# Performance work log

Measured on AMD Instinct MI355X. Metric: run time of the kernel, lower is better.

## Reference

```python
import jax, jax.numpy as jnp
import numpy as np

B, NS, NT = 4, 512, 512
D_IN, C1, R, C2 = 128, 64, 32, 32
E = 32768
STEPS = 10


def setup_inputs() -> dict:
    key = jax.random.key(0)
    ks = jax.random.split(key, 12)
    inp = {}
    inp['x_s'] = jax.random.normal(ks[0], (B * NS, D_IN), jnp.float32)
    inp['edge_index_s'] = jax.random.randint(ks[1], (2, E), 0, B * NS, jnp.int32)
    inp['edge_attr_s'] = jax.random.uniform(ks[2], (E,), jnp.float32)
    inp['batch_s'] = (jnp.arange(B * NS, dtype=jnp.int32) // NS)
    inp['x_t'] = jax.random.normal(ks[3], (B * NT, D_IN), jnp.float32)
    inp['edge_index_t'] = jax.random.randint(ks[4], (2, E), 0, B * NT, jnp.int32)
    inp['edge_attr_t'] = jax.random.uniform(ks[5], (E,), jnp.float32)
    inp['batch_t'] = (jnp.arange(B * NT, dtype=jnp.int32) // NT)
    inp['W1'] = jax.random.normal(ks[6], (D_IN, C1), jnp.float32) / np.float32(np.sqrt(D_IN))
    inp['W2'] = jax.random.normal(ks[7], (R, C2), jnp.float32) / np.float32(np.sqrt(R))
    inp['mw1'] = jax.random.normal(ks[8], (C2, C2), jnp.float32) / np.float32(np.sqrt(C2))
    inp['mb1'] = jnp.zeros((C2,), jnp.float32)
    inp['mw2'] = jax.random.normal(ks[9], (C2, 1), jnp.float32) / np.float32(np.sqrt(C2))
    inp['mb2'] = jnp.zeros((1,), jnp.float32)
    inp['r'] = jax.random.normal(ks[10], (STEPS, B, NS, R), jnp.float32)
    return inp


def psi(x, src, dst, ea, W, n):
    # simple message-passing GNN: edge-weighted neighbor aggregation + linear + ReLU
    m = jax.ops.segment_sum(x[src] * ea[:, None], dst, num_segments=n)
    return jax.nn.relu((x + m) @ W)


def reference(x_s, edge_index_s, edge_attr_s, batch_s, x_t, edge_index_t, edge_attr_t,
              batch_t, W1, W2, mw1, mb1, mw2, mb2, r):
    # Uniform graph sizes -> to_dense_batch is a reshape and all masks are True,
    # so masked_softmax reduces to plain softmax; batch_s/batch_t kept for interface fidelity.
    ss, ds = edge_index_s[0], edge_index_s[1]
    st, dt = edge_index_t[0], edge_index_t[1]
    h_s = psi(x_s, ss, ds, edge_attr_s, W1, B * NS).reshape(B, NS, C1)
    h_t = psi(x_t, st, dt, edge_attr_t, W1, B * NT).reshape(B, NT, C1)
    S_hat0 = jnp.einsum('bsc,btc->bst', h_s, h_t)  # [B, NS, NT]
    S_0 = jax.nn.softmax(S_hat0, axis=-1)

    def step(S_hat, r_i):
        S = jax.nn.softmax(S_hat, axis=-1)
        r_t = jnp.einsum('bst,bsr->btr', S, r_i)  # S^T @ r_s
        o_s = psi(r_i.reshape(B * NS, R), ss, ds, edge_attr_s, W2, B * NS).reshape(B, NS, C2)
        o_t = psi(r_t.reshape(B * NT, R), st, dt, edge_attr_t, W2, B * NT).reshape(B, NT, C2)
        Dm = o_s[:, :, None, :] - o_t[:, None, :, :]  # [B, NS, NT, C2] outer difference
        upd = (jax.nn.relu(Dm @ mw1 + mb1) @ mw2 + mb2)[..., 0]
        return S_hat + upd, None

    S_hat, _ = jax.lax.scan(step, S_hat0, r)
    S_L = jax.nn.softmax(S_hat, axis=-1)
    return (S_0, S_L)
```

## Files before the change

kernel.cpp:

```cpp
#include <hip/hip_runtime.h>


constexpr int kB = 4;
constexpr int kNS = 512;
constexpr int kNT = 512;
constexpr int kDin = 128;
constexpr int kC1 = 64;
constexpr int kR = 32;
constexpr int kC2 = 32;
constexpr int kE = 32768;
constexpr int kSteps = 10;
constexpr int kN = kB * kNS;
constexpr int kEP = kE + 16 * kN;
constexpr int kChunkStride = kR * kN;

__global__ void k_hist(const int* __restrict__ ei_s, const int* __restrict__ ei_t,
                       int* __restrict__ deg) {
  int g = blockIdx.y;
  const int* dst = (g ? ei_t : ei_s) + kE;
  int e = blockIdx.x * 256 + threadIdx.x;
  atomicAdd(&deg[g * kN + dst[e]], 1);
}

__global__ void k_scan(const int* __restrict__ deg, int* __restrict__ off,
                       int* __restrict__ cur) {
  int g = blockIdx.x;
  const int* d = deg + g * kN;
  int* o = off + g * (kN + 1);
  int* c = cur + g * kN;
  __shared__ int sums[256];
  int tid = threadIdx.x;
  int loc[8];
  int s = 0;
#pragma unroll
  for (int i = 0; i < 8; ++i) {
    loc[i] = (d[tid * 8 + i] + 15) & ~15;
    s += loc[i];
  }
  sums[tid] = s;
  __syncthreads();
  for (int st = 1; st < 256; st <<= 1) {
    int v = (tid >= st) ? sums[tid - st] : 0;
    __syncthreads();
    sums[tid] += v;
    __syncthreads();
  }
  int base = (tid > 0) ? sums[tid - 1] : 0;
#pragma unroll
  for (int i = 0; i < 8; ++i) {
    int idx = tid * 8 + i;
    o[idx] = base;
    c[idx] = base;
    base += loc[i];
  }
  if (tid == 255) o[kN] = base;
}

__global__ void k_scatter(const int* __restrict__ ei_s, const int* __restrict__ ei_t,
                          const float* __restrict__ ea_s, const float* __restrict__ ea_t,
                          int* __restrict__ cur, int* __restrict__ srcs,
                          float* __restrict__ eaw) {
  int g = blockIdx.y;
  const int* ei = g ? ei_t : ei_s;
  const float* ea = g ? ea_t : ea_s;
  int e = blockIdx.x * 256 + threadIdx.x;
  int d = ei[kE + e];
  int srcv = ei[e];
  int pos = atomicAdd(&cur[g * kN + d], 1);
  srcs[g * kEP + pos] = srcv;
  eaw[g * kEP + pos] = ea[e];
}

__device__ __forceinline__ void psi2_node(
    int n, const float* __restrict__ vin, const int* __restrict__ sr,
    const float* __restrict__ ew, const int* __restrict__ o,
    const float* __restrict__ W2, const float* __restrict__ mw1,
    const float* __restrict__ mb1, float* __restrict__ Pout) {
  int lane = threadIdx.x & 63;
  int f = lane & 31, hh = lane >> 5;
  int beg = o[n], end = o[n + 1];
  float m = 0.f;
  for (int b0 = beg + hh * 8; b0 < end; b0 += 16) {
#pragma unroll
    for (int q = 0; q < 8; ++q)
      m += vin[(size_t)sr[b0 + q] * kR + f] * ew[b0 + q];
  }
  m += __shfl_down(m, 32, 64);
  float v = vin[(size_t)n * kR + f] + m;
  float acc = 0.f;
#pragma unroll
  for (int k = 0; k < kC2; ++k) acc += __shfl(v, k, 64) * W2[k * kC2 + f];
  float ov = fmaxf(acc, 0.f);
  float p = mb1 ? mb1[f] : 0.f;
#pragma unroll
  for (int k = 0; k < kC2; ++k) p += __shfl(ov, k, 64) * mw1[k * kC2 + f];
  if (lane < 32) Pout[(size_t)n * kC2 + f] = p;
}

__global__ __launch_bounds__(256) void k_pre(
    const float* __restrict__ x_s, const float* __restrict__ x_t,
    const float* __restrict__ r, const int* __restrict__ srcs,
    const float* __restrict__ eaw, const int* __restrict__ off,
    const float* __restrict__ W1, const float* __restrict__ W2,
    const float* __restrict__ mw1, const float* __restrict__ mb1,
    float* __restrict__ h, float* __restrict__ PsAll) {
  int bid = blockIdx.x, tid = threadIdx.x;
  if (bid < 2048) {
    int g = bid >> 10;
    int n = (bid & 1023) * 2 + (tid >> 7);
    int f = tid & 127;
    const float* x = g ? x_t : x_s;
    const int* sr = srcs + g * kEP;
    const float* ew = eaw + g * kEP;
    const int* o = off + g * (kN + 1);
    float* ho = h + (size_t)g * kN * kC1;
    __shared__ float y[2][kDin];
    int beg = o[n], end = o[n + 1];
    float xself = x[(size_t)n * kDin + f];
    float m = 0.f;
    for (int idx = beg; idx < end; idx += 8) {
      float a0 = x[(size_t)sr[idx + 0] * kDin + f] * ew[idx + 0];
      float a1 = x[(size_t)sr[idx + 1] * kDin + f] * ew[idx + 1];
      float a2 = x[(size_t)sr[idx + 2] * kDin + f] * ew[idx + 2];
      float a3 = x[(size_t)sr[idx + 3] * kDin + f] * ew[idx + 3];
      float a4 = x[(size_t)sr[idx + 4] * kDin + f] * ew[idx + 4];
      float a5 = x[(size_t)sr[idx + 5] * kDin + f] * ew[idx + 5];
      float a6 = x[(size_t)sr[idx + 6] * kDin + f] * ew[idx + 6];
      float a7 = x[(size_t)sr[idx + 7] * kDin + f] * ew[idx + 7];
      m += ((a0 + a1) + (a2 + a3)) + ((a4 + a5) + (a6 + a7));
    }
    y[tid >> 7][f] = xself + m;
    __syncthreads();
    if (f < kC1) {
      const float* yy = y[tid >> 7];
      float acc = 0.f;
#pragma unroll 16
      for (int k = 0; k < kDin; ++k) acc += yy[k] * W1[k * kC1 + f];
      ho[(size_t)n * kC1 + f] = fmaxf(acc, 0.f);
    }
  } else {
    int nn = (bid - 2048) * 4 + (tid >> 6);
    int step = nn >> 11, node = nn & (kN - 1);
    psi2_node(node, r + (size_t)step * kN * kR, srcs, eaw, off, W2, mw1, mb1,
              PsAll + (size_t)step * kN * kR);
  }
}

__global__ __launch_bounds__(256) void k_shat0(const float* __restrict__ h,
                                               float* __restrict__ Shat,
                                               float* __restrict__ pstatm,
                                               float* __restrict__ pstatl) {
  int b = blockIdx.z, s0 = blockIdx.y * 64, t0 = blockIdx.x * 64;
  const float* hs = h + (size_t)(b * kNS + s0) * kC1;
  const float* ht = h + (size_t)kN * kC1 + (size_t)(b * kNT + t0) * kC1;
  __shared__ float As[64 * 68];
  __shared__ float Bs[64 * 68];
  int tid = threadIdx.x;
#pragma unroll
  for (int k2 = 0; k2 < 4; ++k2) {
    int idx = tid + k2 * 256;
    int row = idx >> 4, c4 = idx & 15;
    float4 va = *(const float4*)(hs + (size_t)row * kC1 + c4 * 4);
    *(float4*)&As[row * 68 + c4 * 4] = va;
    float4 vb = *(const float4*)(ht + (size_t)row * kC1 + c4 * 4);
    *(float4*)&Bs[row * 68 + c4 * 4] = vb;
  }
  __syncthreads();
  int ts = tid >> 4, tt = tid & 15;
  float acc[4][4] = {};
#pragma unroll
  for (int cc = 0; cc < 16; ++cc) {
    float4 a[4], bt[4];
#pragma unroll
    for (int i = 0; i < 4; ++i) a[i] = *(const float4*)&As[(ts * 4 + i) * 68 + cc * 4];
#pragma unroll
    for (int k = 0; k < 4; ++k) bt[k] = *(const float4*)&Bs[(tt + 16 * k) * 68 + cc * 4];
#pragma unroll
    for (int i = 0; i < 4; ++i)
#pragma unroll
      for (int k = 0; k < 4; ++k)
        acc[i][k] += a[i].x * bt[k].x + a[i].y * bt[k].y + a[i].z * bt[k].z + a[i].w * bt[k].w;
  }
#pragma unroll
  for (int i = 0; i < 4; ++i) {
    int s = s0 + ts * 4 + i;
    float* row = Shat + (size_t)(b * kNS + s) * kNT;
#pragma unroll
    for (int k = 0; k < 4; ++k) row[t0 + tt + 16 * k] = acc[i][k];
  }
#pragma unroll
  for (int i = 0; i < 4; ++i) {
    float mm = fmaxf(fmaxf(acc[i][0], acc[i][1]), fmaxf(acc[i][2], acc[i][3]));
#pragma unroll
    for (int o2 = 8; o2; o2 >>= 1) mm = fmaxf(mm, __shfl_xor(mm, o2, 64));
    float se = 0.f;
#pragma unroll
    for (int k = 0; k < 4; ++k) se += __expf(acc[i][k] - mm);
#pragma unroll
    for (int o2 = 8; o2; o2 >>= 1) se += __shfl_xor(se, o2, 64);
    if (tt == 0) {
      int grow = b * kNS + s0 + ts * 4 + i;
      pstatm[blockIdx.x * kN + grow] = mm;
      pstatl[blockIdx.x * kN + grow] = se;
    }
  }
}

__global__ __launch_bounds__(256) void k_rt(const float* __restrict__ Shat,
                                            const float* __restrict__ pstatm,
                                            const float* __restrict__ pstatl,
                                            const float* __restrict__ ri,
                                            float* __restrict__ part, int nc,
                                            float* __restrict__ Sout) {
  int b = blockIdx.z, cs = blockIdx.y, s0 = cs * 64, t0 = blockIdx.x * 32;
  __shared__ float Wt[64 * 32];
  __shared__ float rch[64 * 32];
  __shared__ float lm[64], ll[64];
  int tid = threadIdx.x;
  if (tid < 64) {
    int row = b * kNS + s0 + tid;
    float m = -3.4e38f;
    for (int c = 0; c < nc; ++c) m = fmaxf(m, pstatm[c * kN + row]);
    float l = 0.f;
    for (int c = 0; c < nc; ++c) l += __expf(pstatm[c * kN + row] - m) * pstatl[c * kN + row];
    lm[tid] = m;
    ll[tid] = 1.f / l;
  }
  __syncthreads();
#pragma unroll
  for (int k2 = 0; k2 < 2; ++k2) {
    int idx = tid + k2 * 256;
    int row = idx >> 3, c4 = idx & 7;
    int grow = b * kNS + s0 + row;
    float4 v = *(const float4*)(Shat + (size_t)grow * kNT + t0 + c4 * 4);
    float m = lm[row], l = ll[row];
    float4 wv;
    wv.x = __expf(v.x - m) * l;
    wv.y = __expf(v.y - m) * l;
    wv.z = __expf(v.z - m) * l;
    wv.w = __expf(v.w - m) * l;
    *(float4*)&Wt[row * 32 + c4 * 4] = wv;
    if (Sout) *(float4*)(Sout + (size_t)grow * kNT + t0 + c4 * 4) = wv;
    float4 rv = *(const float4*)(ri + (size_t)grow * kR + c4 * 4);
    *(float4*)&rch[row * 32 + c4 * 4] = rv;
  }
  __syncthreads();
  int t_l = tid & 31, jg = tid >> 5;
  float4 acc = make_float4(0.f, 0.f, 0.f, 0.f);
  for (int s = 0; s < 64; ++s) {
    float wv = Wt[s * 32 + t_l];
    float4 rv = *(const float4*)&rch[s * 32 + jg * 4];
    acc.x += wv * rv.x; acc.y += wv * rv.y; acc.z += wv * rv.z; acc.w += wv * rv.w;
  }
  int gcol = b * kNT + t0 + t_l;
  float* dst = part + (size_t)cs * kChunkStride + (size_t)jg * 4 * kN + gcol;
  dst[0] = acc.x;
  dst[(size_t)kN] = acc.y;
  dst[(size_t)2 * kN] = acc.z;
  dst[(size_t)3 * kN] = acc.w;
}

__global__ __launch_bounds__(256) void k_red(const float* __restrict__ part,
                                             float* __restrict__ rt) {
  int idx = blockIdx.x * 256 + threadIdx.x;
  int j = idx >> 11, col = idx & (kN - 1);
  float s = 0.f;
#pragma unroll
  for (int cs = 0; cs < 8; ++cs) s += part[(size_t)cs * kChunkStride + idx];
  rt[(size_t)col * kR + j] = s;
}

__global__ __launch_bounds__(256) void k_psi2t(
    const float* __restrict__ rt, const int* __restrict__ srcs,
    const float* __restrict__ eaw, const int* __restrict__ off,
    const float* __restrict__ W2, const float* __restrict__ mw1,
    float* __restrict__ Pt) {
  int n = blockIdx.x * 4 + (threadIdx.x >> 6);
  psi2_node(n, rt, srcs + kEP, eaw + kEP, off + (kN + 1), W2, mw1, nullptr, Pt);
}

__global__ __launch_bounds__(256) void k_upd(
    float* __restrict__ Shat, const float* __restrict__ Ps,
    const float* __restrict__ Pt, const float* __restrict__ mw2,
    const float* __restrict__ mb2, float* __restrict__ pstatm,
    float* __restrict__ pstatl) {
  __shared__ float pts[256 * 33];
  __shared__ float red[8 * 4];
  __shared__ float lmx[8];
  int tid = threadIdx.x;
  int g0 = blockIdx.x * 8;
  int cc = blockIdx.y;
  int bb = g0 >> 9;
  int c0 = cc * 256;
  const float4* PtB = (const float4*)(Pt + ((size_t)bb * kNT + c0) * kC2);
#pragma unroll
  for (int k = 0; k < 8; ++k) {
    int idx = tid + k * 256;
    int col = idx >> 3, q = idx & 7;
    float4 v = PtB[idx];
    float* d = &pts[col * 33 + q * 4];
    d[0] = v.x; d[1] = v.y; d[2] = v.z; d[3] = v.w;
  }
  float old[8];
#pragma unroll
  for (int s = 0; s < 8; ++s) old[s] = Shat[(size_t)(g0 + s) * kNT + c0 + tid];
  __syncthreads();
  float pt[32];
#pragma unroll
  for (int j = 0; j < 32; ++j) pt[j] = pts[tid * 33 + j];
  float bias = mb2[0];
  float nv[8];
#pragma unroll
  for (int s = 0; s < 8; ++s) {
    const float* psr = Ps + (size_t)(g0 + s) * kC2;
    float u = 0.f;
#pragma unroll
    for (int j = 0; j < 32; ++j) u += fmaxf(psr[j] - pt[j], 0.f) * mw2[j];
    float v = old[s] + u + bias;
    Shat[(size_t)(g0 + s) * kNT + c0 + tid] = v;
    nv[s] = v;
  }
  int wv = tid >> 6, ln = tid & 63;
#pragma unroll
  for (int s = 0; s < 8; ++s) {
    float m = nv[s];
#pragma unroll
    for (int o2 = 32; o2; o2 >>= 1) m = fmaxf(m, __shfl_down(m, o2, 64));
    if (ln == 0) red[s * 4 + wv] = m;
  }
  __syncthreads();
  if (tid < 8) {
    lmx[tid] = fmaxf(fmaxf(red[tid * 4], red[tid * 4 + 1]),
                     fmaxf(red[tid * 4 + 2], red[tid * 4 + 3]));
  }
  __syncthreads();
#pragma unroll
  for (int s = 0; s < 8; ++s) {
    float e = __expf(nv[s] - lmx[s]);
#pragma unroll
    for (int o2 = 32; o2; o2 >>= 1) e += __shfl_down(e, o2, 64);
    if (ln == 0) red[s * 4 + wv] = e;
  }
  __syncthreads();
  if (tid < 8) {
    float l = red[tid * 4] + red[tid * 4 + 1] + red[tid * 4 + 2] + red[tid * 4 + 3];
    pstatm[cc * kN + g0 + tid] = lmx[tid];
    pstatl[cc * kN + g0 + tid] = l;
  }
}

__global__ __launch_bounds__(256) void k_out(const float* __restrict__ Shat,
                                             const float* __restrict__ pstatm,
                                             const float* __restrict__ pstatl,
                                             float* __restrict__ out) {
  int row = blockIdx.x, tid = threadIdx.x;
  float m0 = pstatm[row], m1 = pstatm[kN + row];
  float l0 = pstatl[row], l1 = pstatl[kN + row];
  float m = fmaxf(m0, m1);
  float linv = 1.f / (__expf(m0 - m) * l0 + __expf(m1 - m) * l1);
  const float* p = Shat + (size_t)row * kNT;
  float* d = out + (size_t)row * kNT;
  d[tid] = __expf(p[tid] - m) * linv;
  d[tid + 256] = __expf(p[tid + 256] - m) * linv;
}

extern "C" void kernel_launch(void* const* d_in, const int* in_sizes, int n_in,
                              void* d_out, int out_size, void* d_ws, size_t ws_size,
                              hipStream_t stream) {
  (void)in_sizes; (void)n_in; (void)out_size; (void)ws_size;
  const float* x_s = (const float*)d_in[0];
  const int* ei_s = (const int*)d_in[1];
  const float* ea_s = (const float*)d_in[2];
  const float* x_t = (const float*)d_in[4];
  const int* ei_t = (const int*)d_in[5];
  const float* ea_t = (const float*)d_in[6];
  const float* W1 = (const float*)d_in[8];
  const float* W2 = (const float*)d_in[9];
  const float* mw1 = (const float*)d_in[10];
  const float* mb1 = (const float*)d_in[11];
  const float* mw2 = (const float*)d_in[12];
  const float* mb2 = (const float*)d_in[13];
  const float* r = (const float*)d_in[14];
  float* out = (float*)d_out;

  char* w = (char*)d_ws;
  auto alloc = [&](size_t bytes) -> void* {
    void* p = (void*)w;
    w += (bytes + 255) & ~(size_t)255;
    return p;
  };
  int* deg = (int*)alloc((size_t)2 * kN * 4);
  int* cur = (int*)alloc((size_t)2 * kN * 4);
  int* srcs = (int*)alloc((size_t)2 * kEP * 4);
  float* eaw = (float*)alloc((size_t)2 * kEP * 4);
  size_t zbytes = (size_t)((char*)(eaw + 2 * kEP) - (char*)deg);
  int* off = (int*)alloc((size_t)2 * (kN + 1) * 4);
  float* h = (float*)alloc((size_t)2 * kN * kC1 * 4);
  float* Shat = (float*)alloc((size_t)kB * kNS * kNT * 4);
  float* pstatm = (float*)alloc((size_t)8 * kN * 4);
  float* pstatl = (float*)alloc((size_t)8 * kN * 4);
  float* rt = (float*)alloc((size_t)kN * kR * 4);
  float* PsAll = (float*)alloc((size_t)kSteps * kN * kR * 4);
  float* Pt = (float*)alloc((size_t)kN * kC2 * 4);
  float* part = (float*)alloc((size_t)8 * kChunkStride * 4);

  hipMemsetAsync(deg, 0, zbytes, stream);
  k_hist<<<dim3(kE / 256, 2), 256, 0, stream>>>(ei_s, ei_t, deg);
  k_scan<<<2, 256, 0, stream>>>(deg, off, cur);
  k_scatter<<<dim3(kE / 256, 2), 256, 0, stream>>>(ei_s, ei_t, ea_s, ea_t, cur, srcs, eaw);
  k_pre<<<7168, 256, 0, stream>>>(x_s, x_t, r, srcs, eaw, off, W1, W2, mw1, mb1,
                                  h, PsAll);
  k_shat0<<<dim3(8, 8, kB), 256, 0, stream>>>(h, Shat, pstatm, pstatl);
  k_rt<<<dim3(16, 8, kB), 256, 0, stream>>>(Shat, pstatm, pstatl, r, part, 8, out);
  k_red<<<kChunkStride / 256, 256, 0, stream>>>(part, rt);
  for (int i = 0; i < kSteps; ++i) {
    k_psi2t<<<kN / 4, 256, 0, stream>>>(rt, srcs, eaw, off, W2, mw1, Pt);
    k_upd<<<dim3(kN / 8, 2), 256, 0, stream>>>(Shat, PsAll + (size_t)i * kN * kR, Pt,
                                               mw2, mb2, pstatm, pstatl);
    if (i + 1 < kSteps) {
      k_rt<<<dim3(16, 8, kB), 256, 0, stream>>>(Shat, pstatm, pstatl,
                                                r + (size_t)(i + 1) * kN * kR, part,
                                                2, nullptr);
      k_red<<<kChunkStride / 256, 256, 0, stream>>>(part, rt);
    }
  }
  k_out<<<kN, 256, 0, stream>>>(Shat, pstatm, pstatl, out + (size_t)kB * kNS * kNT);
}
```

Baseline: 425.7 us.

## Fuse partial reduction into k_rt via last-block counter and simplify relu-diff update

```diff
diff --git a/kernel.cpp b/kernel.cpp
--- a/kernel.cpp
+++ b/kernel.cpp
@@ -75,7 +75,8 @@
     int n, const float* __restrict__ vin, const int* __restrict__ sr,
     const float* __restrict__ ew, const int* __restrict__ o,
     const float* __restrict__ W2, const float* __restrict__ mw1,
-    const float* __restrict__ mb1, float* __restrict__ Pout) {
+    const float* __restrict__ mb1, const float* __restrict__ mw2w,
+    float* __restrict__ Pout, float* __restrict__ ctOut) {
   int lane = threadIdx.x & 63;
   int f = lane & 31, hh = lane >> 5;
   int beg = o[n], end = o[n + 1];
@@ -95,6 +96,12 @@
 #pragma unroll
   for (int k = 0; k < kC2; ++k) p += __shfl(ov, k, 64) * mw1[k * kC2 + f];
   if (lane < 32) Pout[(size_t)n * kC2 + f] = p;
+  if (ctOut) {
+    float c = p * mw2w[f];
+#pragma unroll
+    for (int o2 = 16; o2; o2 >>= 1) c += __shfl_xor(c, o2, 64);
+    if (lane == 0) ctOut[n] = c;
+  }
 }
 
 __global__ __launch_bounds__(256) void k_pre(
@@ -142,7 +149,7 @@
     int nn = (bid - 2048) * 4 + (tid >> 6);
     int step = nn >> 11, node = nn & (kN - 1);
     psi2_node(node, r + (size_t)step * kN * kR, srcs, eaw, off, W2, mw1, mb1,
-              PsAll + (size_t)step * kN * kR);
+              nullptr, PsAll + (size_t)step * kN * kR, nullptr);
   }
 }
 
@@ -211,11 +218,14 @@
                                             const float* __restrict__ pstatl,
                                             const float* __restrict__ ri,
                                             float* __restrict__ part, int nc,
-                                            float* __restrict__ Sout) {
+                                            float* __restrict__ Sout,
+                                            float* __restrict__ rt,
+                                            int* __restrict__ cnt) {
   int b = blockIdx.z, cs = blockIdx.y, s0 = cs * 64, t0 = blockIdx.x * 32;
   __shared__ float Wt[64 * 32];
   __shared__ float rch[64 * 32];
   __shared__ float lm[64], ll[64];
+  __shared__ int s_last;
   int tid = threadIdx.x;
   if (tid < 64) {
     int row = b * kNS + s0 + tid;
@@ -258,32 +268,41 @@
   dst[(size_t)kN] = acc.y;
   dst[(size_t)2 * kN] = acc.z;
   dst[(size_t)3 * kN] = acc.w;
-}
-
-__global__ __launch_bounds__(256) void k_red(const float* __restrict__ part,
-                                             float* __restrict__ rt) {
-  int idx = blockIdx.x * 256 + threadIdx.x;
-  int j = idx >> 11, col = idx & (kN - 1);
-  float s = 0.f;
-#pragma unroll
-  for (int cs = 0; cs < 8; ++cs) s += part[(size_t)cs * kChunkStride + idx];
-  rt[(size_t)col * kR + j] = s;
+  __threadfence();
+  __syncthreads();
+  if (tid == 0) s_last = (atomicAdd(&cnt[b * 16 + blockIdx.x], 1) == 7);
+  __syncthreads();
+  if (s_last) {
+    __threadfence();
+    for (int u = tid; u < 1024; u += 256) {
+      int j = u >> 5, cl = u & 31;
+      int gc = b * kNT + t0 + cl;
+      size_t idx = (size_t)j * kN + gc;
+      float s = 0.f;
+#pragma unroll
+      for (int c2 = 0; c2 < 8; ++c2) s += part[(size_t)c2 * kChunkStride + idx];
+      rt[(size_t)gc * kR + j] = s;
+    }
+    if (tid == 0) cnt[b * 16 + blockIdx.x] = 0;
+  }
 }
 
 __global__ __launch_bounds__(256) void k_psi2t(
     const float* __restrict__ rt, const int* __restrict__ srcs,
     const float* __restrict__ eaw, const int* __restrict__ off,
     const float* __restrict__ W2, const float* __restrict__ mw1,
-    float* __restrict__ Pt) {
+    const float* __restrict__ mw2, float* __restrict__ Pt,
+    float* __restrict__ ct) {
   int n = blockIdx.x * 4 + (threadIdx.x >> 6);
-  psi2_node(n, rt, srcs + kEP, eaw + kEP, off + (kN + 1), W2, mw1, nullptr, Pt);
+  psi2_node(n, rt, srcs + kEP, eaw + kEP, off + (kN + 1), W2, mw1, nullptr,
+            mw2, Pt, ct);
 }
 
 __global__ __launch_bounds__(256) void k_upd(
     float* __restrict__ Shat, const float* __restrict__ Ps,
-    const float* __restrict__ Pt, const float* __restrict__ mw2,
-    const float* __restrict__ mb2, float* __restrict__ pstatm,
-    float* __restrict__ pstatl) {
+    const float* __restrict__ Pt, const float* __restrict__ ctb,
+    const float* __restrict__ mw2, const float* __restrict__ mb2,
+    float* __restrict__ pstatm, float* __restrict__ pstatl) {
   __shared__ float pts[256 * 33];
   __shared__ float red[8 * 4];
   __shared__ float lmx[8];
@@ -304,18 +323,19 @@
   float old[8];
 #pragma unroll
   for (int s = 0; s < 8; ++s) old[s] = Shat[(size_t)(g0 + s) * kNT + c0 + tid];
+  float ctv = ctb[(size_t)bb * kNT + c0 + tid];
   __syncthreads();
   float pt[32];
 #pragma unroll
   for (int j = 0; j < 32; ++j) pt[j] = pts[tid * 33 + j];
-  float bias = mb2[0];
+  float bias = mb2[0] - ctv;
   float nv[8];
 #pragma unroll
   for (int s = 0; s < 8; ++s) {
     const float* psr = Ps + (size_t)(g0 + s) * kC2;
     float u = 0.f;
 #pragma unroll
-    for (int j = 0; j < 32; ++j) u += fmaxf(psr[j] - pt[j], 0.f) * mw2[j];
+    for (int j = 0; j < 32; ++j) u += fmaxf(psr[j], pt[j]) * mw2[j];
     float v = old[s] + u + bias;
     Shat[(size_t)(g0 + s) * kNT + c0 + tid] = v;
     nv[s] = v;
@@ -391,6 +411,7 @@
   };
   int* deg = (int*)alloc((size_t)2 * kN * 4);
   int* cur = (int*)alloc((size_t)2 * kN * 4);
+  int* cnt = (int*)alloc((size_t)64 * 4);
   int* srcs = (int*)alloc((size_t)2 * kEP * 4);
   float* eaw = (float*)alloc((size_t)2 * kEP * 4);
   size_t zbytes = (size_t)((char*)(eaw + 2 * kEP) - (char*)deg);
@@ -402,6 +423,7 @@
   float* rt = (float*)alloc((size_t)kN * kR * 4);
   float* PsAll = (float*)alloc((size_t)kSteps * kN * kR * 4);
   float* Pt = (float*)alloc((size_t)kN * kC2 * 4);
+  float* ct = (float*)alloc((size_t)kN * 4);
   float* part = (float*)alloc((size_t)8 * kChunkStride * 4);
 
   hipMemsetAsync(deg, 0, zbytes, stream);
@@ -411,17 +433,16 @@
   k_pre<<<7168, 256, 0, stream>>>(x_s, x_t, r, srcs, eaw, off, W1, W2, mw1, mb1,
                                   h, PsAll);
   k_shat0<<<dim3(8, 8, kB), 256, 0, stream>>>(h, Shat, pstatm, pstatl);
-  k_rt<<<dim3(16, 8, kB), 256, 0, stream>>>(Shat, pstatm, pstatl, r, part, 8, out);
-  k_red<<<kChunkStride / 256, 256, 0, stream>>>(part, rt);
+  k_rt<<<dim3(16, 8, kB), 256, 0, stream>>>(Shat, pstatm, pstatl, r, part, 8,
+                                            out, rt, cnt);
   for (int i = 0; i < kSteps; ++i) {
-    k_psi2t<<<kN / 4, 256, 0, stream>>>(rt, srcs, eaw, off, W2, mw1, Pt);
-    k_upd<<<dim3(kN / 8, 2), 256, 0, stream>>>(Shat, PsAll + (size_t)i * kN * kR, Pt,
-                                               mw2, mb2, pstatm, pstatl);
+    k_psi2t<<<kN / 4, 256, 0, stream>>>(rt, srcs, eaw, off, W2, mw1, mw2, Pt, ct);
+    k_upd<<<dim3(kN / 8, 2), 256, 0, stream>>>(Shat, PsAll + (size_t)i * kN * kR,
+                                               Pt, ct, mw2, mb2, pstatm, pstatl);
     if (i + 1 < kSteps) {
       k_rt<<<dim3(16, 8, kB), 256, 0, stream>>>(Shat, pstatm, pstatl,
                                                 r + (size_t)(i + 1) * kN * kR, part,
-                                                2, nullptr);
-      k_red<<<kChunkStride / 256, 256, 0, stream>>>(part, rt);
+                                                2, nullptr, rt, cnt);
     }
   }
   k_out<<<kN, 256, 0, stream>>>(Shat, pstatm, pstatl, out + (size_t)kB * kNS * kNT);
```

Measured after the change: 874.8 us. +105.5%, slower.
